# Kernel optimization log

Hardware: AMD Instinct MI355X
Metric: run time of the kernel (lower is better)

The kernel has to match this reference:

```python
import jax, jax.numpy as jnp
import numpy as np


def setup_inputs() -> dict:
    key = jax.random.key(0)
    ks = jax.random.split(key, 8)
    dim, E = 128, 8
    b, t, h, w = 2, 16, 64, 64
    scale = 1.0 / np.sqrt(dim)
    return {
        "x": jax.random.normal(ks[0], (b, dim, t, h, w), jnp.float32),
        "gate_w": jax.random.normal(ks[1], (dim, E), jnp.float32) * scale,
        "gate_b": jax.random.normal(ks[2], (E,), jnp.float32) * 0.01,
        "W1": jax.random.normal(ks[3], (E, dim, dim), jnp.float32) * scale,
        "b1": jax.random.normal(ks[4], (E, dim), jnp.float32) * 0.01,
        "alpha": jnp.full((E,), 0.25, jnp.float32),  # PReLU default init
        "W2": jax.random.normal(ks[5], (E, dim, dim), jnp.float32) * scale,
        "b2": jax.random.normal(ks[6], (E, dim), jnp.float32) * 0.01,
        "top_k": 2,
    }


def reference(x, gate_w, gate_b, W1, b1, alpha, W2, b2, top_k):
    b, c, t, h, w = x.shape
    E = gate_w.shape[1]
    # tokens: [N, c] with N = b*t*h*w (matches permute(0,2,3,4,1).reshape(-1,c))
    xf = jnp.transpose(x, (0, 2, 3, 4, 1)).reshape(-1, c)
    N = xf.shape[0]
    logits = xf @ gate_w + gate_b                      # [N, E]
    vals, idx = jax.lax.top_k(logits, top_k)           # [N, K]
    probs = jax.nn.softmax(vals, axis=1)               # softmax over selected logits
    # scatter combine weights to dense [N, E] (zero for unselected experts)
    combine = jnp.zeros((N, E), xf.dtype).at[jnp.arange(N)[:, None], idx].add(probs)
    # expert MLP (1x1x1 conv == per-token linear), scalar PReLU per expert
    h1 = jnp.einsum('nc,eoc->eno', xf, W1) + b1[:, None, :]          # [E, N, c]
    h1 = jnp.maximum(h1, 0) + alpha[:, None, None] * jnp.minimum(h1, 0)
    h2 = jnp.einsum('eno,epo->enp', h1, W2) + b2[:, None, :]         # [E, N, c]
    out = jnp.einsum('ne,enc->nc', combine, h2)                      # weighted combine
    out = jnp.transpose(out.reshape(b, t, h, w, c), (0, 4, 1, 2, 3))
    return out + x
```

## Files before the change

### kernel.cpp

```cpp
#include <hip/hip_runtime.h>

typedef float f32x4  __attribute__((ext_vector_type(4)));
typedef float f32x16 __attribute__((ext_vector_type(16)));
typedef __bf16 bf16x8 __attribute__((ext_vector_type(8)));

#define SPAT 65536
#define CH   128
#define NE   8

#define XT_OFF    0
#define OA_OFF    65536
#define OA_ROWB   272
#define B1_OFF    135440
#define B2_OFF    139536
#define SLT_OFF   143632
#define SLC_OFF   145680
#define DSC_OFF   149776
#define CNT_OFF   149904
#define AL_OFF    150096
#define NG_OFF    150128
#define LDS_BYTES 150144

static __device__ __forceinline__ unsigned short bf(float f) {
    __bf16 h = (__bf16)f; return __builtin_bit_cast(unsigned short, h);
}
static __device__ __forceinline__ unsigned pk2(float a, float b) {
    return (unsigned)bf(a) | ((unsigned)bf(b) << 16);
}
static __device__ __forceinline__ float ub(unsigned short u) {
    return __builtin_bit_cast(float, (unsigned)u << 16);
}

__global__ void conv_w(const float* __restrict__ W1, const float* __restrict__ W2,
                       unsigned char* __restrict__ wimg) {
    const int gid = blockIdx.x * 256 + threadIdx.x;
    const int mat = gid >> 14;
    const int e   = (gid >> 11) & 7;
    const int r   = (gid >> 4) & 127;
    const int p   = gid & 15;
    int src_row = r;
    if (mat == 0) {
        const int n = 4 * (r >> 5) + ((r >> 3) & 3);
        src_row = (n >> 1) * 16 + ((r >> 2) & 1) * 8 + (n & 1) * 4 + (r & 3);
    }
    const float* s = (mat ? W2 : W1) + (e * 16384 + src_row * 128 + p * 8);
    uint4 pk;
    pk.x = pk2(s[0], s[1]); pk.y = pk2(s[2], s[3]);
    pk.z = pk2(s[4], s[5]); pk.w = pk2(s[6], s[7]);
    *(uint4*)(wimg + mat * 262144 + e * 32768 + r * 256 + p * 16) = pk;
}

template<bool ADD>
static __device__ __forceinline__ void group_body(
        unsigned char* smem, const unsigned char* __restrict__ wimg,
        int g, int l31, int hi)
{
    const unsigned desc = ((const unsigned*)(smem + DSC_OFF))[g];
    const int e  = (int)(desc >> 16);
    const int s  = (int)(desc & 0xFFFFu) + l31;
    const unsigned tokRaw = ((const unsigned short*)(smem + SLT_OFF))[s];
    const float ce = ((const float*)(smem + SLC_OFF))[s];
    const int tokx  = (int)(tokRaw & 255u);
    const int rowOA = (tokRaw > 255u) ? 256 : (int)tokRaw;
    const float alph = ((const float*)(smem + AL_OFF))[e];

    uint4 xb[8];
    #pragma unroll
    for (int kc = 0; kc < 8; ++kc)
        xb[kc] = *(const uint4*)(smem + XT_OFF + tokx * 256
                                  + (((2 * kc + hi) ^ (tokx & 15)) * 16));

    const unsigned char* W1i = wimg + e * 32768;
    const unsigned char* W2i = wimg + 262144 + e * 32768;

    f32x16 D[4] = {};
    #pragma unroll 1
    for (int gt = 0; gt < 4; ++gt) {
        uint4 a1[8];
        #pragma unroll
        for (int kc = 0; kc < 8; ++kc)
            a1[kc] = *(const uint4*)(W1i + (gt * 32 + l31) * 256 + (2 * kc + hi) * 16);
        f32x16 h0 = {}, h1 = {};
        #pragma unroll
        for (int kc = 0; kc < 4; ++kc) {
            h0 = __builtin_amdgcn_mfma_f32_32x32x16_bf16(
                    __builtin_bit_cast(bf16x8, a1[2 * kc]),
                    __builtin_bit_cast(bf16x8, xb[2 * kc]), h0, 0, 0, 0);
            h1 = __builtin_amdgcn_mfma_f32_32x32x16_bf16(
                    __builtin_bit_cast(bf16x8, a1[2 * kc + 1]),
                    __builtin_bit_cast(bf16x8, xb[2 * kc + 1]), h1, 0, 0, 0);
        }
        uint4 pa2[2];
        #pragma unroll
        for (int q = 0; q < 4; ++q) {
            const int n = 4 * gt + q, kt2 = n >> 1, half = n & 1;
            const int obase = kt2 * 16 + hi * 8 + half * 4;
            const f32x4 b1v = *(const f32x4*)(smem + B1_OFF + e * 512 + obase * 4);
            float hv[4];
            #pragma unroll
            for (int i = 0; i < 4; ++i) {
                float z = h0[q * 4 + i] + h1[q * 4 + i] + b1v[i];
                z = fmaxf(z, 0.f) + alph * fminf(z, 0.f);
                hv[i] = z * ce;
            }
            ((unsigned*)&pa2[q >> 1])[half * 2]     = pk2(hv[0], hv[1]);
            ((unsigned*)&pa2[q >> 1])[half * 2 + 1] = pk2(hv[2], hv[3]);
        }
        #pragma unroll
        for (int dk = 0; dk < 2; ++dk) {
            const int kt2 = 2 * gt + dk;
            #pragma unroll
            for (int n2 = 0; n2 < 4; ++n2) {
                const uint4 wf = *(const uint4*)(W2i + (n2 * 32 + l31) * 256
                                                  + (2 * kt2 + hi) * 16);
                D[n2] = __builtin_amdgcn_mfma_f32_32x32x16_bf16(
                        __builtin_bit_cast(bf16x8, wf),
                        __builtin_bit_cast(bf16x8, pa2[dk]), D[n2], 0, 0, 0);
            }
        }
    }
    unsigned char* oarow = smem + OA_OFF + rowOA * OA_ROWB;
    #pragma unroll
    for (int n2 = 0; n2 < 4; ++n2) {
        #pragma unroll
        for (int q = 0; q < 4; ++q) {
            const int p0 = n2 * 32 + q * 8 + hi * 4;
            const f32x4 b2v = *(const f32x4*)(smem + B2_OFF + e * 512 + p0 * 4);
            float vv[4];
            #pragma unroll
            for (int i = 0; i < 4; ++i) vv[i] = D[n2][q * 4 + i] + ce * b2v[i];
            uint2* dst = (uint2*)(oarow + p0 * 2);
            if (ADD) {
                const uint2 old = *dst;
                vv[0] += ub((unsigned short)(old.x & 0xFFFFu));
                vv[1] += ub((unsigned short)(old.x >> 16));
                vv[2] += ub((unsigned short)(old.y & 0xFFFFu));
                vv[3] += ub((unsigned short)(old.y >> 16));
            }
            uint2 nw; nw.x = pk2(vv[0], vv[1]); nw.y = pk2(vv[2], vv[3]);
            *dst = nw;
        }
    }
}

__global__ __launch_bounds__(512) __attribute__((amdgpu_waves_per_eu(2, 2)))
void moe_main(const float* __restrict__ x,  const float* __restrict__ gw,
              const float* __restrict__ gb, const float* __restrict__ b1,
              const float* __restrict__ alpha, const float* __restrict__ b2,
              const unsigned char* __restrict__ wimg, float* __restrict__ out)
{
    __shared__ __align__(16) unsigned char smem[LDS_BYTES];
    const int t = threadIdx.x, lane = t & 63, w = t >> 6, blk = blockIdx.x;
    const int l31 = lane & 31, hi = lane >> 5;
    const size_t xbase = (size_t)(blk >> 8) * (size_t)(CH * SPAT) + (size_t)((blk & 255) << 8);
    const int m = w * 32 + l31;
    unsigned* C = (unsigned*)(smem + CNT_OFF);

    if (t < 48) C[t] = 0;
    if (t < 256)      ((f32x4*)(smem + B1_OFF))[t]       = ((const f32x4*)b1)[t];
    else              ((f32x4*)(smem + B2_OFF))[t - 256] = ((const f32x4*)b2)[t - 256];
    if (t < 8) ((float*)(smem + AL_OFF))[t] = alpha[t];

    f32x4 plo = {0.f,0.f,0.f,0.f}, phi = {0.f,0.f,0.f,0.f};
    #pragma unroll
    for (int kc = 0; kc < 8; ++kc) {
        const int c0 = kc * 16 + hi * 8;
        float v8[8];
        #pragma unroll
        for (int j = 0; j < 8; ++j) v8[j] = x[xbase + (size_t)(c0 + j) * SPAT + m];
        #pragma unroll
        for (int j = 0; j < 8; ++j) {
            const f32x4 g0 = *(const f32x4*)(gw + (c0 + j) * NE);
            const f32x4 g1 = *(const f32x4*)(gw + (c0 + j) * NE + 4);
            plo += v8[j] * g0; phi += v8[j] * g1;
        }
        uint4 pkv;
        pkv.x = pk2(v8[0], v8[1]); pkv.y = pk2(v8[2], v8[3]);
        pkv.z = pk2(v8[4], v8[5]); pkv.w = pk2(v8[6], v8[7]);
        *(uint4*)(smem + XT_OFF + m * 256 + (((2 * kc + hi) ^ (m & 15)) * 16)) = pkv;
    }
    #pragma unroll
    for (int i2 = 0; i2 < 4; ++i2) {
        plo[i2] += __shfl_xor(plo[i2], 32, 64);
        phi[i2] += __shfl_xor(phi[i2], 32, 64);
    }
    int i0, i1; float q0, q1;
    {
        float lg[8];
        #pragma unroll
        for (int e2 = 0; e2 < 4; ++e2) { lg[e2] = plo[e2] + gb[e2]; lg[4 + e2] = phi[e2] + gb[4 + e2]; }
        i0 = 0; float v0 = lg[0];
        #pragma unroll
        for (int e2 = 1; e2 < 8; ++e2) if (lg[e2] > v0) { v0 = lg[e2]; i0 = e2; }
        i1 = -1; float v1 = -3.4e38f;
        #pragma unroll
        for (int e2 = 0; e2 < 8; ++e2) if (e2 != i0 && lg[e2] > v1) { v1 = lg[e2]; i1 = e2; }
        const float d = expf(v1 - v0);
        q0 = 1.f / (1.f + d);
        q1 = d   / (1.f + d);
    }
    __syncthreads();

    if (hi == 0) {
        atomicAdd(&C[i0], 1u);
        atomicAdd(&C[8 + i1], 1u);
    }
    __syncthreads();

    if (t == 0) {
        unsigned* dsc = (unsigned*)(smem + DSC_OFF);
        int ng = 0; unsigned base = 0;
        for (int e = 0; e < 8; ++e) {
            const unsigned c = C[e], gc = (c + 31) >> 5;
            C[16 + e] = base; C[32 + e] = base;
            for (unsigned k = 0; k < gc; ++k) dsc[ng++] = ((unsigned)e << 16) | (base + k * 32);
            base += gc * 32;
        }
        ((int*)(smem + NG_OFF))[0] = ng;
        for (int e = 0; e < 8; ++e) {
            const unsigned c = C[8 + e], gc = (c + 31) >> 5;
            C[24 + e] = base; C[40 + e] = base;
            for (unsigned k = 0; k < gc; ++k) dsc[ng++] = ((unsigned)e << 16) | (base + k * 32);
            base += gc * 32;
        }
        ((int*)(smem + NG_OFF))[1] = ng;
    }
    __syncthreads();

    if (hi == 0) {
        const unsigned pP = atomicAdd(&C[16 + i0], 1u);
        ((unsigned short*)(smem + SLT_OFF))[pP] = (unsigned short)m;
        ((float*)(smem + SLC_OFF))[pP] = q0;
        const unsigned pQ = atomicAdd(&C[24 + i1], 1u);
        ((unsigned short*)(smem + SLT_OFF))[pQ] = (unsigned short)m;
        ((float*)(smem + SLC_OFF))[pQ] = q1;
    }
    __syncthreads();

    if (t < 16) {
        const int e = t & 7;
        const unsigned c  = (t < 8) ? C[e] : C[8 + e];
        const unsigned bs = (t < 8) ? C[32 + e] : C[40 + e];
        const unsigned en = bs + ((c + 31) & ~31u);
        for (unsigned s2 = bs + c; s2 < en; ++s2) {
            ((unsigned short*)(smem + SLT_OFF))[s2] = 0xFFFFu;
            ((float*)(smem + SLC_OFF))[s2] = 0.f;
        }
    }
    __syncthreads();

    const int NGP = ((const int*)(smem + NG_OFF))[0];
    const int NGT = ((const int*)(smem + NG_OFF))[1];

    #pragma unroll 1
    for (int g = w; g < NGP; g += 8) group_body<false>(smem, wimg, g, l31, hi);
    __syncthreads();
    #pragma unroll 1
    for (int g = NGP + w; g < NGT; g += 8) group_body<true>(smem, wimg, g, l31, hi);
    __syncthreads();

    {
        const int etok = t & 255;
        const int gb8  = (t >> 8) * 8;
        const unsigned char* oarow = smem + OA_OFF + etok * OA_ROWB;
        #pragma unroll
        for (int gi = 0; gi < 8; ++gi) {
            const int gran = gb8 + gi;
            const uint4 r = *(const uint4*)(oarow + gran * 16);
            const unsigned short* u = (const unsigned short*)&r;
            #pragma unroll
            for (int j = 0; j < 8; ++j) {
                const int p = gran * 8 + j;
                const size_t a = xbase + (size_t)p * SPAT + etok;
                out[a] = ub(u[j]) + x[a];
            }
        }
    }
}

extern "C" void kernel_launch(void* const* d_in, const int* in_sizes, int n_in,
                              void* d_out, int out_size, void* d_ws, size_t ws_size,
                              hipStream_t stream) {
    const float* x  = (const float*)d_in[0];
    const float* gw = (const float*)d_in[1];
    const float* gb = (const float*)d_in[2];
    const float* W1 = (const float*)d_in[3];
    const float* b1 = (const float*)d_in[4];
    const float* al = (const float*)d_in[5];
    const float* W2 = (const float*)d_in[6];
    const float* b2 = (const float*)d_in[7];
    (void)in_sizes; (void)n_in; (void)out_size; (void)ws_size;
    unsigned char* wimg = (unsigned char*)d_ws;
    float* out = (float*)d_out;

    conv_w<<<dim3(128), dim3(256), 0, stream>>>(W1, W2, wimg);
    moe_main<<<dim3(512), dim3(512), 0, stream>>>(x, gw, gb, b1, al, b2, wimg, out);
}
```

Baseline: 139.6 us.

## Split expert MLP into two phases and assign contiguous group ranges per wave

The group body now computes all first-layer activations into a full register array first, then runs the second-layer MFMA loop fully unrolled, batching four weight loads ahead of each set of MFMAs. This is meant to remove the serial dependency between the layer-1 epilogue and layer-2 MFMAs and to expose more load/MFMA overlap, at the cost of higher register pressure from the unrolled loops and the 8-entry activation array. Group scheduling also changes from strided (g += 8) to contiguous per-wave ranges, which alters locality of expert weight accesses and how work is balanced across waves.

Result: slower. 160.0 us (+14.6%).

```diff
diff --git a/kernel.cpp b/kernel.cpp
--- a/kernel.cpp
+++ b/kernel.cpp
@@ -73,8 +73,8 @@
     const unsigned char* W1i = wimg + e * 32768;
     const unsigned char* W2i = wimg + 262144 + e * 32768;
 
-    f32x16 D[4] = {};
-    #pragma unroll 1
+    uint4 pa[8];
+    #pragma unroll
     for (int gt = 0; gt < 4; ++gt) {
         uint4 a1[8];
         #pragma unroll
@@ -90,10 +90,9 @@
                     __builtin_bit_cast(bf16x8, a1[2 * kc + 1]),
                     __builtin_bit_cast(bf16x8, xb[2 * kc + 1]), h1, 0, 0, 0);
         }
-        uint4 pa2[2];
         #pragma unroll
         for (int q = 0; q < 4; ++q) {
-            const int n = 4 * gt + q, kt2 = n >> 1, half = n & 1;
+            const int kt2 = 2 * gt + (q >> 1), half = q & 1;
             const int obase = kt2 * 16 + hi * 8 + half * 4;
             const f32x4 b1v = *(const f32x4*)(smem + B1_OFF + e * 512 + obase * 4);
             float hv[4];
@@ -103,22 +102,25 @@
                 z = fmaxf(z, 0.f) + alph * fminf(z, 0.f);
                 hv[i] = z * ce;
             }
-            ((unsigned*)&pa2[q >> 1])[half * 2]     = pk2(hv[0], hv[1]);
-            ((unsigned*)&pa2[q >> 1])[half * 2 + 1] = pk2(hv[2], hv[3]);
-        }
-        #pragma unroll
-        for (int dk = 0; dk < 2; ++dk) {
-            const int kt2 = 2 * gt + dk;
-            #pragma unroll
-            for (int n2 = 0; n2 < 4; ++n2) {
-                const uint4 wf = *(const uint4*)(W2i + (n2 * 32 + l31) * 256
-                                                  + (2 * kt2 + hi) * 16);
-                D[n2] = __builtin_amdgcn_mfma_f32_32x32x16_bf16(
-                        __builtin_bit_cast(bf16x8, wf),
-                        __builtin_bit_cast(bf16x8, pa2[dk]), D[n2], 0, 0, 0);
-            }
-        }
-    }
+            ((unsigned*)&pa[kt2])[half * 2]     = pk2(hv[0], hv[1]);
+            ((unsigned*)&pa[kt2])[half * 2 + 1] = pk2(hv[2], hv[3]);
+        }
+    }
+
+    f32x16 D[4] = {};
+    #pragma unroll
+    for (int kt2 = 0; kt2 < 8; ++kt2) {
+        uint4 wf[4];
+        #pragma unroll
+        for (int n2 = 0; n2 < 4; ++n2)
+            wf[n2] = *(const uint4*)(W2i + (n2 * 32 + l31) * 256 + (2 * kt2 + hi) * 16);
+        #pragma unroll
+        for (int n2 = 0; n2 < 4; ++n2)
+            D[n2] = __builtin_amdgcn_mfma_f32_32x32x16_bf16(
+                    __builtin_bit_cast(bf16x8, wf[n2]),
+                    __builtin_bit_cast(bf16x8, pa[kt2]), D[n2], 0, 0, 0);
+    }
+
     unsigned char* oarow = smem + OA_OFF + rowOA * OA_ROWB;
     #pragma unroll
     for (int n2 = 0; n2 < 4; ++n2) {
@@ -252,11 +254,18 @@
     const int NGP = ((const int*)(smem + NG_OFF))[0];
     const int NGT = ((const int*)(smem + NG_OFF))[1];
 
-    #pragma unroll 1
-    for (int g = w; g < NGP; g += 8) group_body<false>(smem, wimg, g, l31, hi);
-    __syncthreads();
-    #pragma unroll 1
-    for (int g = NGP + w; g < NGT; g += 8) group_body<true>(smem, wimg, g, l31, hi);
+    {
+        const int g0 = (w * NGP) >> 3, g1 = ((w + 1) * NGP) >> 3;
+        #pragma unroll 1
+        for (int g = g0; g < g1; ++g) group_body<false>(smem, wimg, g, l31, hi);
+    }
+    __syncthreads();
+    {
+        const int ns = NGT - NGP;
+        const int g0 = NGP + ((w * ns) >> 3), g1 = NGP + (((w + 1) * ns) >> 3);
+        #pragma unroll 1
+        for (int g = g0; g < g1; ++g) group_body<true>(smem, wimg, g, l31, hi);
+    }
     __syncthreads();
 
     {
```
